# Performance work log

Measured on AMD Instinct MI355X. Metric: run time of the kernel, lower is better.

The kernel has to match this reference:

```python
import jax, jax.numpy as jnp
import numpy as np

NEG = -1e9  # stand-in for -inf in masked_fill; avoids NaN rows for never-gathered states


def _residual(x, w1, b1, w2, b2):
    # ResidualLayerOld: two relu linears with a residual connection (eval mode, no dropout)
    h = jax.nn.relu(x @ w1.T + b1)
    return x + jax.nn.relu(h @ w2.T + b2)


def setup_inputs() -> dict:
    key = jax.random.key(0)
    B, T, V, C, H, SPW = 16, 256, 32000, 1024, 512, 8
    ks = jax.random.split(key, 32)
    s = 0.05  # keep logits in a sane range
    inp = {
        'start_emb': jax.random.normal(ks[0], (C, H), jnp.float32) * s,
        'start_l1w': jax.random.normal(ks[1], (H, H), jnp.float32) * s,
        'start_l1b': jnp.zeros((H,), jnp.float32),
        'start_l2w': jax.random.normal(ks[2], (H, H), jnp.float32) * s,
        'start_l2b': jnp.zeros((H,), jnp.float32),
        'start_ow': jax.random.normal(ks[3], (1, H), jnp.float32) * s,
        'start_ob': jnp.zeros((1,), jnp.float32),
        'state_emb': jax.random.normal(ks[4], (C, H), jnp.float32) * s,
        'trans_l1w': jax.random.normal(ks[5], (H, H), jnp.float32) * s,
        'trans_l1b': jnp.zeros((H,), jnp.float32),
        'trans_l2w': jax.random.normal(ks[6], (H, H), jnp.float32) * s,
        'trans_l2b': jnp.zeros((H,), jnp.float32),
        'proj_w': jax.random.normal(ks[7], (C, H), jnp.float32) * s,
        'pret_emb': jax.random.normal(ks[8], (C, H), jnp.float32) * s,
        'term_l1w': jax.random.normal(ks[9], (H, H), jnp.float32) * s,
        'term_l1b': jnp.zeros((H,), jnp.float32),
        'term_l2w': jax.random.normal(ks[10], (H, H), jnp.float32) * s,
        'term_l2b': jnp.zeros((H,), jnp.float32),
        'term_ow': jax.random.normal(ks[11], (V, H), jnp.float32) * s,
        'term_ob': jnp.zeros((V,), jnp.float32),
        'text': jax.random.randint(ks[12], (B, T), 0, V, jnp.int32),
        'word2state': jax.random.randint(ks[13], (V, SPW), 0, C, jnp.int32),
    }
    return inp


def reference(start_emb, start_l1w, start_l1b, start_l2w, start_l2b, start_ow, start_ob,
              state_emb, trans_l1w, trans_l1b, trans_l2w, trans_l2b, proj_w,
              pret_emb, term_l1w, term_l1b, term_l2w, term_l2b, term_ow, term_ob,
              text, word2state):
    C, H = start_emb.shape
    V, SPW = word2state.shape

    # start: MLP(C,H)->(C,1) -> log_softmax over C
    start = jax.nn.log_softmax(
        (_residual(start_emb, start_l1w, start_l1b, start_l2w, start_l2b) @ start_ow.T + start_ob).squeeze(-1))

    # transition: [C,C] log_softmax over next state
    trans = jax.nn.log_softmax(
        _residual(state_emb, trans_l1w, trans_l1b, trans_l2w, trans_l2b) @ proj_w.T, axis=-1)

    # emission: [C,V] logits, masked to the sparse word->state assignment, log_softmax over V
    term_logits = _residual(pret_emb, term_l1w, term_l1b, term_l2w, term_l2b) @ term_ow.T + term_ob
    mask = jnp.zeros((C, V), bool).at[word2state.reshape(-1), jnp.repeat(jnp.arange(V), SPW)].set(True)
    emission = jax.nn.log_softmax(jnp.where(mask, term_logits, NEG), axis=-1)

    # clamp: gather per-timestep [SPW,SPW] transition blocks + emissions
    cs = word2state[text]                               # [B,T,SPW]
    pot = trans[cs[:, :-1, :, None], cs[:, 1:, None, :]]  # [B,T-1,SPW,SPW] (prev i, next j)
    init = start[cs[:, 0]]                              # [B,SPW]
    obs = emission[cs, text[:, :, None]]                # [B,T,SPW]
    pot = pot.at[:, 0].add((init + obs[:, 0])[:, :, None])
    pot = pot + obs[:, 1:][:, :, None, :]               # add obs_{t+1} along next-state j
    pot = jnp.swapaxes(pot, -1, -2)                     # [B,T-1,next,prev], as in clamp()

    # forward algorithm (fb kernel's alpha pass): alpha_{t+1}[n] = LSE_p pot[t,n,p] + alpha_t[p]
    def step(alpha, p):
        a = jax.nn.logsumexp(p + alpha[:, None, :], axis=-1)
        return a, None

    B = text.shape[0]
    alpha0 = jnp.zeros((B, SPW), pot.dtype)
    alphaT, _ = jax.lax.scan(step, alpha0, jnp.swapaxes(pot, 0, 1))
    evidence = jax.nn.logsumexp(alphaT, axis=-1).sum()  # full-length sequences
    return evidence
```

## Files before the change

### kernel.cpp

```cpp
#include <hip/hip_runtime.h>
#include <hip/hip_bf16.h>

#define C_DIM 1024
#define H_DIM 512
#define V_DIM 32000
#define B_DIM 16
#define T_DIM 256
#define SPW   8
#define NSLOT 32
#define NSEG  32

typedef unsigned short u16;
typedef unsigned int   u32;
typedef __attribute__((ext_vector_type(8))) short bf16x8;
typedef __attribute__((ext_vector_type(4))) float f32x4;

__device__ __forceinline__ u16 f2b(float f) {
    union { float f; u32 i; } x; x.f = f;
    u32 i = x.i;
    i += 0x7fffu + ((i >> 16) & 1u);
    return (u16)(i >> 16);
}
__device__ __forceinline__ float b2f(u16 u) {
    union { u32 i; float f; } x; x.i = ((u32)u) << 16; return x.f;
}
__device__ __forceinline__ float dot8_bf16(uint4 u, const float4 tw0, const float4 tw1) {
    return tw0.x * b2f((u16)(u.x & 0xffff)) + tw0.y * b2f((u16)(u.x >> 16))
         + tw0.z * b2f((u16)(u.y & 0xffff)) + tw0.w * b2f((u16)(u.y >> 16))
         + tw1.x * b2f((u16)(u.z & 0xffff)) + tw1.y * b2f((u16)(u.z >> 16))
         + tw1.z * b2f((u16)(u.w & 0xffff)) + tw1.w * b2f((u16)(u.w >> 16));
}

struct CvtArgs {
    const float* src[6];
    u16*         dst[6];
    int          n[6];
    float*       zero;
    int          zn;
    float*       out;
};

__global__ __launch_bounds__(256) void cvt_kern(CvtArgs a)
{
    int seg = blockIdx.y;
    if (seg == 6) {
        for (int i = blockIdx.x * 256 + threadIdx.x; i < a.zn; i += gridDim.x * 256)
            a.zero[i] = 0.0f;
        if (blockIdx.x == 0 && threadIdx.x == 0) a.out[0] = 0.0f;
        return;
    }
    const float4* s = (const float4*)a.src[seg];
    ushort4* d = (ushort4*)a.dst[seg];
    int n4 = a.n[seg] >> 2;
    for (int i = blockIdx.x * 256 + threadIdx.x; i < n4; i += gridDim.x * 256) {
        float4 v = s[i];
        ushort4 o;
        o.x = f2b(v.x); o.y = f2b(v.y); o.z = f2b(v.z); o.w = f2b(v.w);
        d[i] = o;
    }
}

struct MlpArgs {
    const u16*   A[3];
    const u16*   W[3];
    const float* bias[3];
    const float* resid[3];
    u16*         out[3];
    const float* csrc[4];
    u16*         cdst[4];
    int          cn[4];
};

__global__ __launch_bounds__(256) void mlp16_kern(MlpArgs args)
{
    if (blockIdx.z == 3) {
        int idx = (blockIdx.y * gridDim.x + blockIdx.x) * 256 + threadIdx.x;
        int stride = gridDim.x * gridDim.y * 256;
#pragma unroll
        for (int s = 0; s < 4; s++) {
            const float4* sp = (const float4*)args.csrc[s];
            ushort4* dp = (ushort4*)args.cdst[s];
            int n4 = args.cn[s] >> 2;
            for (int t = idx; t < n4; t += stride) {
                float4 v = sp[t];
                ushort4 o;
                o.x = f2b(v.x); o.y = f2b(v.y); o.z = f2b(v.z); o.w = f2b(v.w);
                dp[t] = o;
            }
        }
        return;
    }
    const int N = H_DIM, K = H_DIM;
    int z = blockIdx.z;
    const u16* A = args.A[z];
    const u16* B = args.W[z];
    const float* bias = args.bias[z];
    const float* resid = args.resid[z];
    u16* out = args.out[z];

    __shared__ __align__(16) u16 As[2][64][40];
    __shared__ __align__(16) u16 Bs[2][64][40];
    int tid  = threadIdx.x;
    int m0 = blockIdx.x * 64, n0 = blockIdx.y * 64;
    int wave = tid >> 6, lane = tid & 63;
    int wr = wave >> 1, wc = wave & 1;
    int srow = tid >> 2, scol = (tid & 3) << 3;
    int quad = lane >> 4, l16 = lane & 15;
    f32x4 acc[2][2] = {};

    const u16* ap = A + (size_t)(m0 + srow) * K + scol;
    const u16* bp = B + (size_t)(n0 + srow) * K + scol;

    *(uint4*)&As[0][srow][scol] = *(const uint4*)ap;
    *(uint4*)&Bs[0][srow][scol] = *(const uint4*)bp;
    __syncthreads();
    int cur = 0;
#pragma unroll 1
    for (int k0 = 0; k0 + 32 < K; k0 += 32) {
        uint4 an = *(const uint4*)(ap + k0 + 32);
        uint4 bn = *(const uint4*)(bp + k0 + 32);
        bf16x8 af0 = *(const bf16x8*)&As[cur][wr * 32 + l16][quad * 8];
        bf16x8 af1 = *(const bf16x8*)&As[cur][wr * 32 + 16 + l16][quad * 8];
        bf16x8 bf0 = *(const bf16x8*)&Bs[cur][wc * 32 + l16][quad * 8];
        bf16x8 bf1 = *(const bf16x8*)&Bs[cur][wc * 32 + 16 + l16][quad * 8];
        acc[0][0] = __builtin_amdgcn_mfma_f32_16x16x32_bf16(af0, bf0, acc[0][0], 0, 0, 0);
        acc[0][1] = __builtin_amdgcn_mfma_f32_16x16x32_bf16(af0, bf1, acc[0][1], 0, 0, 0);
        acc[1][0] = __builtin_amdgcn_mfma_f32_16x16x32_bf16(af1, bf0, acc[1][0], 0, 0, 0);
        acc[1][1] = __builtin_amdgcn_mfma_f32_16x16x32_bf16(af1, bf1, acc[1][1], 0, 0, 0);
        *(uint4*)&As[cur ^ 1][srow][scol] = an;
        *(uint4*)&Bs[cur ^ 1][srow][scol] = bn;
        __syncthreads();
        cur ^= 1;
    }
    {
        bf16x8 af0 = *(const bf16x8*)&As[cur][wr * 32 + l16][quad * 8];
        bf16x8 af1 = *(const bf16x8*)&As[cur][wr * 32 + 16 + l16][quad * 8];
        bf16x8 bf0 = *(const bf16x8*)&Bs[cur][wc * 32 + l16][quad * 8];
        bf16x8 bf1 = *(const bf16x8*)&Bs[cur][wc * 32 + 16 + l16][quad * 8];
        acc[0][0] = __builtin_amdgcn_mfma_f32_16x16x32_bf16(af0, bf0, acc[0][0], 0, 0, 0);
        acc[0][1] = __builtin_amdgcn_mfma_f32_16x16x32_bf16(af0, bf1, acc[0][1], 0, 0, 0);
        acc[1][0] = __builtin_amdgcn_mfma_f32_16x16x32_bf16(af1, bf0, acc[1][0], 0, 0, 0);
        acc[1][1] = __builtin_amdgcn_mfma_f32_16x16x32_bf16(af1, bf1, acc[1][1], 0, 0, 0);
    }
#pragma unroll
    for (int sm = 0; sm < 2; sm++)
#pragma unroll
        for (int sn = 0; sn < 2; sn++) {
            int n = n0 + wc * 32 + sn * 16 + l16;
            float bv = bias[n];
#pragma unroll
            for (int reg = 0; reg < 4; reg++) {
                int m = m0 + wr * 32 + sm * 16 + quad * 4 + reg;
                float v = fmaxf(acc[sm][sn][reg] + bv, 0.0f);
                if (resid) v += resid[(size_t)m * N + n];
                out[(size_t)m * N + n] = f2b(v);
            }
        }
}

__global__ __launch_bounds__(256) void fused_mid_kern(
    const u16* __restrict__ Rtrans16, const u16* __restrict__ proj16,
    float* __restrict__ TL, float* __restrict__ rowsum,
    const u16* __restrict__ Rterm16, const float* __restrict__ tow,
    const float* __restrict__ tob, const int* __restrict__ w2s,
    float* __restrict__ Zpart, float* __restrict__ Lmat,
    const u16* __restrict__ Rstart16, const float* __restrict__ sow,
    const float* __restrict__ sob, float* __restrict__ startv,
    float* __restrict__ Ssum)
{
    __shared__ __align__(16) u16 As[2][64][40];
    __shared__ __align__(16) u16 Bs[2][64][40];
    int bx = blockIdx.x;
    int tid = threadIdx.x;
    int wid = tid >> 6, lane = tid & 63;

    if (bx < 256) {
        const int K = H_DIM;
        int m0 = (bx & 15) * 64, n0 = (bx >> 4) * 64;
        int wr = wid >> 1, wc = wid & 1;
        int srow = tid >> 2, scol = (tid & 3) << 3;
        int quad = lane >> 4, l16 = lane & 15;
        f32x4 acc[2][2] = {};

        const u16* ap = Rtrans16 + (size_t)(m0 + srow) * K + scol;
        const u16* bp = proj16 + (size_t)(n0 + srow) * K + scol;

        *(uint4*)&As[0][srow][scol] = *(const uint4*)ap;
        *(uint4*)&Bs[0][srow][scol] = *(const uint4*)bp;
        __syncthreads();
        int cur = 0;
#pragma unroll 1
        for (int k0 = 0; k0 + 32 < K; k0 += 32) {
            uint4 an = *(const uint4*)(ap + k0 + 32);
            uint4 bn = *(const uint4*)(bp + k0 + 32);
            bf16x8 af0 = *(const bf16x8*)&As[cur][wr * 32 + l16][quad * 8];
            bf16x8 af1 = *(const bf16x8*)&As[cur][wr * 32 + 16 + l16][quad * 8];
            bf16x8 bf0 = *(const bf16x8*)&Bs[cur][wc * 32 + l16][quad * 8];
            bf16x8 bf1 = *(const bf16x8*)&Bs[cur][wc * 32 + 16 + l16][quad * 8];
            acc[0][0] = __builtin_amdgcn_mfma_f32_16x16x32_bf16(af0, bf0, acc[0][0], 0, 0, 0);
            acc[0][1] = __builtin_amdgcn_mfma_f32_16x16x32_bf16(af0, bf1, acc[0][1], 0, 0, 0);
            acc[1][0] = __builtin_amdgcn_mfma_f32_16x16x32_bf16(af1, bf0, acc[1][0], 0, 0, 0);
            acc[1][1] = __builtin_amdgcn_mfma_f32_16x16x32_bf16(af1, bf1, acc[1][1], 0, 0, 0);
            *(uint4*)&As[cur ^ 1][srow][scol] = an;
            *(uint4*)&Bs[cur ^ 1][srow][scol] = bn;
            __syncthreads();
            cur ^= 1;
        }
        {
            bf16x8 af0 = *(const bf16x8*)&As[cur][wr * 32 + l16][quad * 8];
            bf16x8 af1 = *(const bf16x8*)&As[cur][wr * 32 + 16 + l16][quad * 8];
            bf16x8 bf0 = *(const bf16x8*)&Bs[cur][wc * 32 + l16][quad * 8];
            bf16x8 bf1 = *(const bf16x8*)&Bs[cur][wc * 32 + 16 + l16][quad * 8];
            acc[0][0] = __builtin_amdgcn_mfma_f32_16x16x32_bf16(af0, bf0, acc[0][0], 0, 0, 0);
            acc[0][1] = __builtin_amdgcn_mfma_f32_16x16x32_bf16(af0, bf1, acc[0][1], 0, 0, 0);
            acc[1][0] = __builtin_amdgcn_mfma_f32_16x16x32_bf16(af1, bf0, acc[1][0], 0, 0, 0);
            acc[1][1] = __builtin_amdgcn_mfma_f32_16x16x32_bf16(af1, bf1, acc[1][1], 0, 0, 0);
        }
#pragma unroll
        for (int sm = 0; sm < 2; sm++)
#pragma unroll
            for (int reg = 0; reg < 4; reg++) {
                int m = m0 + wr * 32 + sm * 16 + quad * 4 + reg;
                float e = 0.0f;
#pragma unroll
                for (int sn = 0; sn < 2; sn++) {
                    int n = n0 + wc * 32 + sn * 16 + l16;
                    float v = acc[sm][sn][reg];
                    TL[(size_t)m * C_DIM + n] = v;
                    e += __expf(v);
                }
                e += __shfl_xor(e, 1, 64);
                e += __shfl_xor(e, 2, 64);
                e += __shfl_xor(e, 4, 64);
                e += __shfl_xor(e, 8, 64);
                if (l16 == 0) atomicAdd(rowsum + m, e);
            }
        return;
    }

    if (bx < 256 + V_DIM / 8) {
        int qbid = bx - 256;
        int slotid = qbid & (NSLOT - 1);
#pragma unroll
        for (int h = 0; h < 2; h++) {
            int v = (qbid * 4 + wid) * 2 + h;
            const float4* twp = (const float4*)(tow + (size_t)v * H_DIM);
            float4 tw0 = twp[lane * 2], tw1 = twp[lane * 2 + 1];
            float ob = tob[v];
            int cs[SPW];
#pragma unroll
            for (int s = 0; s < SPW; s++) cs[s] = w2s[v * SPW + s];
            uint4 rv[SPW];
#pragma unroll
            for (int s = 0; s < SPW; s++)
                rv[s] = ((const uint4*)(Rterm16 + (size_t)cs[s] * H_DIM))[lane];
            float d[SPW];
#pragma unroll
            for (int s = 0; s < SPW; s++) {
                d[s] = dot8_bf16(rv[s], tw0, tw1);
                d[s] += __shfl_xor(d[s], 1, 64);
                d[s] += __shfl_xor(d[s], 2, 64);
                d[s] += __shfl_xor(d[s], 4, 64);
            }
            float x = d[0];
            int myc = cs[0];
#pragma unroll
            for (int s = 1; s < SPW; s++) {
                if ((lane & 7) == s) { x = d[s]; myc = cs[s]; }
            }
            x += __shfl_xor(x, 8, 64);
            x += __shfl_xor(x, 16, 64);
            x += __shfl_xor(x, 32, 64);
            u32 dupmask = 0;
#pragma unroll
            for (int s = 1; s < SPW; s++) {
                bool dp = false;
#pragma unroll
                for (int s2 = 0; s2 < s; s2++) dp = dp || (cs[s2] == cs[s]);
                if (dp) dupmask |= (1u << s);
            }
            if (lane < 8) {
                Lmat[(size_t)v * SPW + lane] = x + ob;
                if (!((dupmask >> lane) & 1u))
                    atomicAdd(Zpart + (size_t)myc * NSLOT + slotid, __expf(x + ob));
            }
        }
        return;
    }

    int sbid = bx - (256 + V_DIM / 8);
    int c = sbid * 4 + wid;
    uint4 rv = ((const uint4*)(Rstart16 + (size_t)c * H_DIM))[lane];
    const float4* wp = (const float4*)(sow);
    float4 w0 = wp[lane * 2], w1 = wp[lane * 2 + 1];
    float d = dot8_bf16(rv, w0, w1);
    for (int off = 1; off < 64; off <<= 1) d += __shfl_xor(d, off, 64);
    if (lane == 0) {
        d += sob[0];
        startv[c] = d;
        atomicAdd(Ssum + (sbid & (NSLOT - 1)), __expf(d));
    }
}

__device__ __forceinline__ float lsm_combine(float accv, float mv, int i, int j)
{
    float x[8];
#pragma unroll
    for (int k = 0; k < 8; k++) {
        float a = __shfl(accv, k * 8 + i, 64);
        float b = __shfl(mv,  j * 8 + k, 64);
        x[k] = a + b;
    }
    float mx = fmaxf(fmaxf(fmaxf(x[0], x[1]), fmaxf(x[2], x[3])),
                     fmaxf(fmaxf(x[4], x[5]), fmaxf(x[6], x[7])));
    float s = 0.0f;
#pragma unroll
    for (int k = 0; k < 8; k++) s += __expf(x[k] - mx);
    return mx + __logf(s);
}

__global__ __launch_bounds__(64) void scanA_kern(
    const float* __restrict__ TL, const float* __restrict__ rowsum,
    const float* __restrict__ Lmat, const float* __restrict__ Zpart,
    const float* __restrict__ startv, const float* __restrict__ Ssum,
    const int* __restrict__ text, const int* __restrict__ w2s,
    float* __restrict__ Mc)
{
    __shared__ float sLZ[C_DIM];
    __shared__ float sLR[C_DIM];
    int lane = threadIdx.x;
    for (int c = lane; c < C_DIM; c += 64) {
        const float4* zp = (const float4*)(Zpart + (size_t)c * NSLOT);
        float4 z0 = zp[0], z1 = zp[1], z2 = zp[2], z3 = zp[3];
        float4 z4 = zp[4], z5 = zp[5], z6 = zp[6], z7 = zp[7];
        float z = ((z0.x + z0.y + z0.z + z0.w) + (z1.x + z1.y + z1.z + z1.w))
                + ((z2.x + z2.y + z2.z + z2.w) + (z3.x + z3.y + z3.z + z3.w))
                + ((z4.x + z4.y + z4.z + z4.w) + (z5.x + z5.y + z5.z + z5.w))
                + ((z6.x + z6.y + z6.z + z6.w) + (z7.x + z7.y + z7.z + z7.w));
        sLZ[c] = __logf(z);
        sLR[c] = __logf(rowsum[c]);
    }
    __syncthreads();

    int g = blockIdx.x;
    int b = g >> 5, c = g & (NSEG - 1);
    int t0 = c * ((T_DIM) / NSEG);
    int cnt = min(T_DIM / NSEG, (T_DIM - 1) - t0);
    int i = lane & 7, j = lane >> 3;

    const int* txt = text + b * T_DIM;

    float logS = 0.0f;
    if (t0 == 0) {
        float ss = 0.0f;
#pragma unroll
        for (int k = 0; k < NSLOT; k++) ss += Ssum[k];
        logS = __logf(ss);
    }

    auto potval = [&](int t) -> float {
        int vt  = txt[t];
        int vt1 = txt[t + 1];
        int ci = w2s[vt * SPW + i];
        int cj = w2s[vt1 * SPW + j];
        float p = TL[(size_t)ci * C_DIM + cj] - sLR[ci]
                + Lmat[(size_t)vt1 * SPW + j] - sLZ[cj];
        if (t == 0)
            p += startv[ci] - logS + Lmat[(size_t)vt * SPW + i] - sLZ[ci];
        return p;
    };

    float acc = potval(t0);
    if (cnt > 1) {
        float nv = potval(t0 + 1);
        for (int t = t0 + 1; t < t0 + cnt; t++) {
            float nv2 = (t + 1 < t0 + cnt) ? potval(t + 1) : 0.0f;
            acc = lsm_combine(acc, nv, i, j);
            nv = nv2;
        }
    }
    Mc[(size_t)g * 64 + lane] = acc;
}

__global__ __launch_bounds__(512) void scanB_kern(const float* __restrict__ Mc,
                                                  float* __restrict__ out)
{
    __shared__ float Lb[8][64];
    int b = blockIdx.x;
    int w = threadIdx.x >> 6, lane = threadIdx.x & 63;
    int i = lane & 7, j = lane >> 3;
    const float* base = Mc + (size_t)b * NSEG * 64;

    float m0 = base[(size_t)(4 * w + 0) * 64 + lane];
    float m1 = base[(size_t)(4 * w + 1) * 64 + lane];
    float m2 = base[(size_t)(4 * w + 2) * 64 + lane];
    float m3 = base[(size_t)(4 * w + 3) * 64 + lane];
    float r01 = lsm_combine(m0, m1, i, j);
    float r23 = lsm_combine(m2, m3, i, j);
    float r = lsm_combine(r01, r23, i, j);
    Lb[w][lane] = r;
    __syncthreads();
    float a, m;
    if (w < 4) { a = Lb[2 * w][lane]; m = Lb[2 * w + 1][lane]; r = lsm_combine(a, m, i, j); }
    __syncthreads();
    if (w < 4) Lb[w][lane] = r;
    __syncthreads();
    if (w < 2) { a = Lb[2 * w][lane]; m = Lb[2 * w + 1][lane]; r = lsm_combine(a, m, i, j); }
    __syncthreads();
    if (w < 2) Lb[w][lane] = r;
    __syncthreads();
    if (w == 0) {
        a = Lb[0][lane]; m = Lb[1][lane];
        r = lsm_combine(a, m, i, j);
        float mx = r;
        for (int o = 1; o < 64; o <<= 1) mx = fmaxf(mx, __shfl_xor(mx, o, 64));
        float e = __expf(r - mx);
        for (int o = 1; o < 64; o <<= 1) e += __shfl_xor(e, o, 64);
        if (lane == 0) atomicAdd(out, mx + __logf(e));
    }
}

extern "C" void kernel_launch(void* const* d_in, const int* in_sizes, int n_in,
                              void* d_out, int out_size, void* d_ws, size_t ws_size,
                              hipStream_t stream)
{
    const float* start_emb = (const float*)d_in[0];
    const float* start_l1w = (const float*)d_in[1];
    const float* start_l1b = (const float*)d_in[2];
    const float* start_l2w = (const float*)d_in[3];
    const float* start_l2b = (const float*)d_in[4];
    const float* start_ow  = (const float*)d_in[5];
    const float* start_ob  = (const float*)d_in[6];
    const float* state_emb = (const float*)d_in[7];
    const float* trans_l1w = (const float*)d_in[8];
    const float* trans_l1b = (const float*)d_in[9];
    const float* trans_l2w = (const float*)d_in[10];
    const float* trans_l2b = (const float*)d_in[11];
    const float* proj_w    = (const float*)d_in[12];
    const float* pret_emb  = (const float*)d_in[13];
    const float* term_l1w  = (const float*)d_in[14];
    const float* term_l1b  = (const float*)d_in[15];
    const float* term_l2w  = (const float*)d_in[16];
    const float* term_l2b  = (const float*)d_in[17];
    const float* term_ow   = (const float*)d_in[18];
    const float* term_ob   = (const float*)d_in[19];
    const int*   text      = (const int*)d_in[20];
    const int*   w2s       = (const int*)d_in[21];

    char* w = (char*)d_ws;
    const u32 MB = 1u << 20;
    const size_t CH = (size_t)C_DIM * H_DIM;
    const size_t HH = (size_t)H_DIM * H_DIM;

    u16*   emb16  = (u16*)(w);
    u16*   w16    = (u16*)(w + 3u * MB);
    u16*   proj16 = (u16*)(w + 6u * MB);
    u16*   H16    = (u16*)(w + 7u * MB);
    u16*   R16    = (u16*)(w + 10u * MB);
    float* TL     = (float*)(w + 13u * MB);
    float* startv = (float*)(w + 17u * MB);
    float* Mc     = (float*)(w + 17u * MB + 4096);
    float* Zpart  = (float*)(w + 18u * MB);
    float* Ssum   = Zpart + (size_t)C_DIM * NSLOT;
    float* rowsum = Ssum + NSLOT;
    float* Lmat   = (float*)(w + 19u * MB);

    u16* semb16 = emb16;
    u16* temb16 = emb16 + CH;
    u16* pemb16 = emb16 + 2 * CH;
    u16* sl1w16 = w16;
    u16* sl2w16 = w16 + HH;
    u16* tl1w16 = w16 + 2 * HH;
    u16* tl2w16 = w16 + 3 * HH;
    u16* ml1w16 = w16 + 4 * HH;
    u16* ml2w16 = w16 + 5 * HH;
    u16* Hs = H16, *Ht = H16 + CH, *Hp = H16 + 2 * CH;
    u16* Rstart16 = R16;
    u16* Rtrans16 = R16 + CH;
    u16* Rterm16  = R16 + 2 * CH;

    dim3 blk256(256);

    CvtArgs cv;
    cv.src[0] = start_emb; cv.dst[0] = semb16; cv.n[0] = (int)CH;
    cv.src[1] = state_emb; cv.dst[1] = temb16; cv.n[1] = (int)CH;
    cv.src[2] = pret_emb;  cv.dst[2] = pemb16; cv.n[2] = (int)CH;
    cv.src[3] = start_l1w; cv.dst[3] = sl1w16; cv.n[3] = (int)HH;
    cv.src[4] = trans_l1w; cv.dst[4] = tl1w16; cv.n[4] = (int)HH;
    cv.src[5] = term_l1w;  cv.dst[5] = ml1w16; cv.n[5] = (int)HH;
    cv.zero = Zpart; cv.zn = C_DIM * NSLOT + NSLOT + C_DIM;
    cv.out = (float*)d_out;
    cvt_kern<<<dim3(64, 7), blk256, 0, stream>>>(cv);

    MlpArgs l1;
    l1.A[0] = semb16; l1.A[1] = temb16; l1.A[2] = pemb16;
    l1.W[0] = sl1w16; l1.W[1] = tl1w16; l1.W[2] = ml1w16;
    l1.bias[0] = start_l1b; l1.bias[1] = trans_l1b; l1.bias[2] = term_l1b;
    l1.resid[0] = nullptr; l1.resid[1] = nullptr; l1.resid[2] = nullptr;
    l1.out[0] = Hs; l1.out[1] = Ht; l1.out[2] = Hp;
    l1.csrc[0] = start_l2w; l1.cdst[0] = sl2w16; l1.cn[0] = (int)HH;
    l1.csrc[1] = trans_l2w; l1.cdst[1] = tl2w16; l1.cn[1] = (int)HH;
    l1.csrc[2] = term_l2w;  l1.cdst[2] = ml2w16; l1.cn[2] = (int)HH;
    l1.csrc[3] = proj_w;    l1.cdst[3] = proj16; l1.cn[3] = (int)CH;

    MlpArgs l2;
    l2.A[0] = Hs; l2.A[1] = Ht; l2.A[2] = Hp;
    l2.W[0] = sl2w16; l2.W[1] = tl2w16; l2.W[2] = ml2w16;
    l2.bias[0] = start_l2b; l2.bias[1] = trans_l2b; l2.bias[2] = term_l2b;
    l2.resid[0] = start_emb; l2.resid[1] = state_emb; l2.resid[2] = pret_emb;
    l2.out[0] = Rstart16; l2.out[1] = Rtrans16; l2.out[2] = Rterm16;
    l2.csrc[0] = nullptr; l2.cdst[0] = nullptr; l2.cn[0] = 0;
    l2.csrc[1] = nullptr; l2.cdst[1] = nullptr; l2.cn[1] = 0;
    l2.csrc[2] = nullptr; l2.cdst[2] = nullptr; l2.cn[2] = 0;
    l2.csrc[3] = nullptr; l2.cdst[3] = nullptr; l2.cn[3] = 0;

    mlp16_kern<<<dim3(16, 8, 4), blk256, 0, stream>>>(l1);
    mlp16_kern<<<dim3(16, 8, 3), blk256, 0, stream>>>(l2);

    fused_mid_kern<<<256 + V_DIM / 8 + C_DIM / 4, blk256, 0, stream>>>(
        Rtrans16, proj16, TL, rowsum,
        Rterm16, term_ow, term_ob, w2s, Zpart, Lmat,
        Rstart16, start_ow, start_ob, startv, Ssum);

    scanA_kern<<<B_DIM * NSEG, dim3(64), 0, stream>>>(TL, rowsum, Lmat, Zpart,
                                                      startv, Ssum, text, w2s, Mc);
    scanB_kern<<<B_DIM, dim3(512), 0, stream>>>(Mc, (float*)d_out);
}
```

Measured before the change: 212.3 us.

## Fuse scan kernels into one per-batch block and interleave two vocab rows

The two forward-scan kernels become a single kernel with one 1024-thread block per batch. Each wave scans two adjacent time segments serially, and the segment results are reduced in shared memory. This removes the intermediate Mc buffer, one kernel launch, and the repeated loading of the log-normaliser tables in every small block, but it uses only 16 blocks, doubles the serial chain per wave and drops the potval prefetch. The emission path in the fused mid kernel now handles two vocab entries side by side to put more independent gathers and shuffles in flight.

```diff
diff --git a/kernel.cpp b/kernel.cpp
--- a/kernel.cpp
+++ b/kernel.cpp
@@ -241,49 +241,60 @@
     if (bx < 256 + V_DIM / 8) {
         int qbid = bx - 256;
         int slotid = qbid & (NSLOT - 1);
-#pragma unroll
-        for (int h = 0; h < 2; h++) {
-            int v = (qbid * 4 + wid) * 2 + h;
-            const float4* twp = (const float4*)(tow + (size_t)v * H_DIM);
-            float4 tw0 = twp[lane * 2], tw1 = twp[lane * 2 + 1];
-            float ob = tob[v];
-            int cs[SPW];
-#pragma unroll
-            for (int s = 0; s < SPW; s++) cs[s] = w2s[v * SPW + s];
-            uint4 rv[SPW];
-#pragma unroll
-            for (int s = 0; s < SPW; s++)
-                rv[s] = ((const uint4*)(Rterm16 + (size_t)cs[s] * H_DIM))[lane];
-            float d[SPW];
-#pragma unroll
-            for (int s = 0; s < SPW; s++) {
-                d[s] = dot8_bf16(rv[s], tw0, tw1);
-                d[s] += __shfl_xor(d[s], 1, 64);
-                d[s] += __shfl_xor(d[s], 2, 64);
-                d[s] += __shfl_xor(d[s], 4, 64);
-            }
-            float x = d[0];
-            int myc = cs[0];
-#pragma unroll
-            for (int s = 1; s < SPW; s++) {
-                if ((lane & 7) == s) { x = d[s]; myc = cs[s]; }
-            }
-            x += __shfl_xor(x, 8, 64);
-            x += __shfl_xor(x, 16, 64);
-            x += __shfl_xor(x, 32, 64);
-            u32 dupmask = 0;
-#pragma unroll
-            for (int s = 1; s < SPW; s++) {
-                bool dp = false;
-#pragma unroll
-                for (int s2 = 0; s2 < s; s2++) dp = dp || (cs[s2] == cs[s]);
-                if (dp) dupmask |= (1u << s);
-            }
-            if (lane < 8) {
-                Lmat[(size_t)v * SPW + lane] = x + ob;
-                if (!((dupmask >> lane) & 1u))
-                    atomicAdd(Zpart + (size_t)myc * NSLOT + slotid, __expf(x + ob));
-            }
+        int v0 = (qbid * 4 + wid) * 2;
+        int v1 = v0 + 1;
+        const float4* twpA = (const float4*)(tow + (size_t)v0 * H_DIM);
+        const float4* twpB = (const float4*)(tow + (size_t)v1 * H_DIM);
+        float4 twA0 = twpA[lane * 2], twA1 = twpA[lane * 2 + 1];
+        float4 twB0 = twpB[lane * 2], twB1 = twpB[lane * 2 + 1];
+        float obA = tob[v0], obB = tob[v1];
+        int csA[SPW], csB[SPW];
+#pragma unroll
+        for (int s = 0; s < SPW; s++) { csA[s] = w2s[v0 * SPW + s]; csB[s] = w2s[v1 * SPW + s]; }
+        uint4 rvA[SPW], rvB[SPW];
+#pragma unroll
+        for (int s = 0; s < SPW; s++)
+            rvA[s] = ((const uint4*)(Rterm16 + (size_t)csA[s] * H_DIM))[lane];
+#pragma unroll
+        for (int s = 0; s < SPW; s++)
+            rvB[s] = ((const uint4*)(Rterm16 + (size_t)csB[s] * H_DIM))[lane];
+        float dA[SPW], dB[SPW];
+#pragma unroll
+        for (int s = 0; s < SPW; s++) {
+            dA[s] = dot8_bf16(rvA[s], twA0, twA1);
+            dB[s] = dot8_bf16(rvB[s], twB0, twB1);
+        }
+#pragma unroll
+        for (int s = 0; s < SPW; s++) {
+            dA[s] += __shfl_xor(dA[s], 1, 64);  dB[s] += __shfl_xor(dB[s], 1, 64);
+            dA[s] += __shfl_xor(dA[s], 2, 64);  dB[s] += __shfl_xor(dB[s], 2, 64);
+            dA[s] += __shfl_xor(dA[s], 4, 64);  dB[s] += __shfl_xor(dB[s], 4, 64);
+        }
+        float xA = dA[0], xB = dB[0];
+        int mycA = csA[0], mycB = csB[0];
+#pragma unroll
+        for (int s = 1; s < SPW; s++) {
+            if ((lane & 7) == s) { xA = dA[s]; mycA = csA[s]; xB = dB[s]; mycB = csB[s]; }
+        }
+        xA += __shfl_xor(xA, 8, 64);   xB += __shfl_xor(xB, 8, 64);
+        xA += __shfl_xor(xA, 16, 64);  xB += __shfl_xor(xB, 16, 64);
+        xA += __shfl_xor(xA, 32, 64);  xB += __shfl_xor(xB, 32, 64);
+        u32 dmA = 0, dmB = 0;
+#pragma unroll
+        for (int s = 1; s < SPW; s++) {
+            bool da = false, db = false;
+#pragma unroll
+            for (int s2 = 0; s2 < s; s2++) { da = da || (csA[s2] == csA[s]); db = db || (csB[s2] == csB[s]); }
+            if (da) dmA |= (1u << s);
+            if (db) dmB |= (1u << s);
+        }
+        if (lane < 8) {
+            Lmat[(size_t)v0 * SPW + lane] = xA + obA;
+            Lmat[(size_t)v1 * SPW + lane] = xB + obB;
+            if (!((dmA >> lane) & 1u))
+                atomicAdd(Zpart + (size_t)mycA * NSLOT + slotid, __expf(xA + obA));
+            if (!((dmB >> lane) & 1u))
+                atomicAdd(Zpart + (size_t)mycB * NSLOT + slotid, __expf(xB + obB));
         }
         return;
     }
@@ -319,17 +330,22 @@
     return mx + __logf(s);
 }
 
-__global__ __launch_bounds__(64) void scanA_kern(
+__global__ __launch_bounds__(1024) void scanAB_kern(
     const float* __restrict__ TL, const float* __restrict__ rowsum,
     const float* __restrict__ Lmat, const float* __restrict__ Zpart,
     const float* __restrict__ startv, const float* __restrict__ Ssum,
     const int* __restrict__ text, const int* __restrict__ w2s,
-    float* __restrict__ Mc)
+    float* __restrict__ out)
 {
     __shared__ float sLZ[C_DIM];
     __shared__ float sLR[C_DIM];
-    int lane = threadIdx.x;
-    for (int c = lane; c < C_DIM; c += 64) {
+    __shared__ float Lw[16][64];
+    int b = blockIdx.x;
+    int tid = threadIdx.x;
+    int wv = tid >> 6, lane = tid & 63;
+
+    {
+        int c = tid;
         const float4* zp = (const float4*)(Zpart + (size_t)c * NSLOT);
         float4 z0 = zp[0], z1 = zp[1], z2 = zp[2], z3 = zp[3];
         float4 z4 = zp[4], z5 = zp[5], z6 = zp[6], z7 = zp[7];
@@ -342,16 +358,11 @@
     }
     __syncthreads();
 
-    int g = blockIdx.x;
-    int b = g >> 5, c = g & (NSEG - 1);
-    int t0 = c * ((T_DIM) / NSEG);
-    int cnt = min(T_DIM / NSEG, (T_DIM - 1) - t0);
     int i = lane & 7, j = lane >> 3;
-
     const int* txt = text + b * T_DIM;
 
     float logS = 0.0f;
-    if (t0 == 0) {
+    if (wv == 0) {
         float ss = 0.0f;
 #pragma unroll
         for (int k = 0; k < NSLOT; k++) ss += Ssum[k];
@@ -370,51 +381,39 @@
         return p;
     };
 
-    float acc = potval(t0);
-    if (cnt > 1) {
-        float nv = potval(t0 + 1);
-        for (int t = t0 + 1; t < t0 + cnt; t++) {
-            float nv2 = (t + 1 < t0 + cnt) ? potval(t + 1) : 0.0f;
-            acc = lsm_combine(acc, nv, i, j);
-            nv = nv2;
-        }
-    }
-    Mc[(size_t)g * 64 + lane] = acc;
-}
-
-__global__ __launch_bounds__(512) void scanB_kern(const float* __restrict__ Mc,
-                                                  float* __restrict__ out)
-{
-    __shared__ float Lb[8][64];
-    int b = blockIdx.x;
-    int w = threadIdx.x >> 6, lane = threadIdx.x & 63;
-    int i = lane & 7, j = lane >> 3;
-    const float* base = Mc + (size_t)b * NSEG * 64;
-
-    float m0 = base[(size_t)(4 * w + 0) * 64 + lane];
-    float m1 = base[(size_t)(4 * w + 1) * 64 + lane];
-    float m2 = base[(size_t)(4 * w + 2) * 64 + lane];
-    float m3 = base[(size_t)(4 * w + 3) * 64 + lane];
-    float r01 = lsm_combine(m0, m1, i, j);
-    float r23 = lsm_combine(m2, m3, i, j);
-    float r = lsm_combine(r01, r23, i, j);
-    Lb[w][lane] = r;
-    __syncthreads();
-    float a, m;
-    if (w < 4) { a = Lb[2 * w][lane]; m = Lb[2 * w + 1][lane]; r = lsm_combine(a, m, i, j); }
-    __syncthreads();
-    if (w < 4) Lb[w][lane] = r;
-    __syncthreads();
-    if (w < 2) { a = Lb[2 * w][lane]; m = Lb[2 * w + 1][lane]; r = lsm_combine(a, m, i, j); }
-    __syncthreads();
-    if (w < 2) Lb[w][lane] = r;
-    __syncthreads();
-    if (w == 0) {
-        a = Lb[0][lane]; m = Lb[1][lane];
-        r = lsm_combine(a, m, i, j);
-        float mx = r;
+    float acc;
+    {
+        int seg = 2 * wv;
+        int t0 = seg * (T_DIM / NSEG);
+        int cnt = min(T_DIM / NSEG, (T_DIM - 1) - t0);
+        acc = potval(t0);
+        for (int t = t0 + 1; t < t0 + cnt; t++)
+            acc = lsm_combine(acc, potval(t), i, j);
+        seg = 2 * wv + 1;
+        t0 = seg * (T_DIM / NSEG);
+        cnt = min(T_DIM / NSEG, (T_DIM - 1) - t0);
+        for (int t = t0; t < t0 + cnt; t++)
+            acc = lsm_combine(acc, potval(t), i, j);
+    }
+    Lw[wv][lane] = acc;
+    __syncthreads();
+    if (wv < 8) { acc = lsm_combine(Lw[2 * wv][lane], Lw[2 * wv + 1][lane], i, j); }
+    __syncthreads();
+    if (wv < 8) Lw[wv][lane] = acc;
+    __syncthreads();
+    if (wv < 4) { acc = lsm_combine(Lw[2 * wv][lane], Lw[2 * wv + 1][lane], i, j); }
+    __syncthreads();
+    if (wv < 4) Lw[wv][lane] = acc;
+    __syncthreads();
+    if (wv < 2) { acc = lsm_combine(Lw[2 * wv][lane], Lw[2 * wv + 1][lane], i, j); }
+    __syncthreads();
+    if (wv < 2) Lw[wv][lane] = acc;
+    __syncthreads();
+    if (wv == 0) {
+        acc = lsm_combine(Lw[0][lane], Lw[1][lane], i, j);
+        float mx = acc;
         for (int o = 1; o < 64; o <<= 1) mx = fmaxf(mx, __shfl_xor(mx, o, 64));
-        float e = __expf(r - mx);
+        float e = __expf(acc - mx);
         for (int o = 1; o < 64; o <<= 1) e += __shfl_xor(e, o, 64);
         if (lane == 0) atomicAdd(out, mx + __logf(e));
     }
@@ -459,7 +458,6 @@
     u16*   R16    = (u16*)(w + 10u * MB);
     float* TL     = (float*)(w + 13u * MB);
     float* startv = (float*)(w + 17u * MB);
-    float* Mc     = (float*)(w + 17u * MB + 4096);
     float* Zpart  = (float*)(w + 18u * MB);
     float* Ssum   = Zpart + (size_t)C_DIM * NSLOT;
     float* rowsum = Ssum + NSLOT;
@@ -522,7 +520,7 @@
         Rterm16, term_ow, term_ob, w2s, Zpart, Lmat,
         Rstart16, start_ow, start_ob, startv, Ssum);
 
-    scanA_kern<<<B_DIM * NSEG, dim3(64), 0, stream>>>(TL, rowsum, Lmat, Zpart,
-                                                      startv, Ssum, text, w2s, Mc);
-    scanB_kern<<<B_DIM, dim3(512), 0, stream>>>(Mc, (float*)d_out);
-}
+    scanAB_kern<<<B_DIM, dim3(1024), 0, stream>>>(TL, rowsum, Lmat, Zpart,
+                                                  startv, Ssum, text, w2s,
+                                                  (float*)d_out);
+}
```

New measurement: 231.0 us. +8.8%, slower.
